# Optimization experiments

Measured on AMD Instinct MI355X. Metric: run time of the kernel, lower is better.

Reference implementation:

```python
import jax, jax.numpy as jnp
import numpy as np
from jax import lax

OBS, ACT, H, VOX = 2264, 32, 4096, 216  # voxel tail is 6*6*6


def _conv3d(v, w, b):
    # v: [1,1,6,6,6], w: [1,1,3,3,3] (OIDHW), SAME padding, stride 1
    y = lax.conv_general_dilated(v, w, window_strides=(1, 1, 1), padding='SAME',
                                 dimension_numbers=('NCDHW', 'OIDHW', 'NCDHW'))
    return jax.nn.relu(y + b.reshape(1, -1, 1, 1, 1))


def setup_inputs() -> dict:
    key = jax.random.key(0)
    ks = jax.random.split(key, 24)
    s = 0.05
    inp = {'x': jax.random.normal(ks[0], (1, OBS), dtype=jnp.float32)}
    # six Conv3d(1,1,3) kernels + biases
    for i in range(6):
        inp[f'cw{i}'] = jax.random.normal(ks[1 + i], (1, 1, 3, 3, 3), dtype=jnp.float32) * s
        inp[f'cb{i}'] = jax.random.normal(ks[7 + i], (1,), dtype=jnp.float32) * s
    # MLP: Linear(OBS->H), Linear(H->H), Linear(H->ACT); torch layout W:[out,in]
    inp['W0'] = jax.random.normal(ks[13], (H, OBS), dtype=jnp.float32) * 0.02
    inp['b0'] = jnp.zeros((H,), jnp.float32)
    inp['W1'] = jax.random.normal(ks[14], (H, H), dtype=jnp.float32) * 0.02
    inp['b1'] = jnp.zeros((H,), jnp.float32)
    inp['W2'] = jax.random.normal(ks[15], (ACT, H), dtype=jnp.float32) * 0.02
    inp['b2'] = jnp.zeros((ACT,), jnp.float32)
    # default transformations (in_shift=0, in_scale=1, out_shift=0, out_scale=1)
    inp['in_shift'] = jnp.zeros((OBS,), jnp.float32)
    inp['in_scale'] = jnp.ones((OBS,), jnp.float32)
    inp['out_shift'] = jnp.zeros((ACT,), jnp.float32)
    inp['out_scale'] = jnp.ones((ACT,), jnp.float32)
    return inp


def reference(x, cw0, cw1, cw2, cw3, cw4, cw5, cb0, cb1, cb2, cb3, cb4, cb5,
              W0, b0, W1, b1, W2, b2, in_shift, in_scale, out_shift, out_scale):
    v = x[:, -VOX:].reshape(1, 1, 6, 6, 6)
    for w, b in ((cw0, cb0), (cw1, cb1), (cw2, cb2), (cw3, cb3), (cw4, cb4), (cw5, cb5)):
        v = _conv3d(v, w, b)
    out = jnp.concatenate([x[:, :-VOX], v.reshape(1, VOX)], axis=1)
    out = (out - in_shift) / (in_scale + 1e-8)
    out = jnp.tanh(out @ W0.T + b0)
    out = jnp.tanh(out @ W1.T + b1)
    out = out @ W2.T + b2
    return out * out_scale + out_shift
```

## Files before the change

### kernel.cpp

```cpp
#include <hip/hip_runtime.h>
#include <math.h>

#define OBS 2264
#define ACT 32
#define HID 4096
#define VOX 216
#define PRE (OBS - VOX)
#define N4_OBS (OBS / 4)
#define N4_HID (HID / 4)
#define NB 256
#define NT 1024
#define RPB 16
#define RPG 4

__global__ __launch_bounds__(NT) void fused0_kernel(
    const float* __restrict__ x,
    const float* __restrict__ cw0, const float* __restrict__ cb0,
    const float* __restrict__ cw1, const float* __restrict__ cb1,
    const float* __restrict__ cw2, const float* __restrict__ cb2,
    const float* __restrict__ cw3, const float* __restrict__ cb3,
    const float* __restrict__ cw4, const float* __restrict__ cb4,
    const float* __restrict__ cw5, const float* __restrict__ cb5,
    const float* __restrict__ in_shift, const float* __restrict__ in_scale,
    const float* __restrict__ W0, const float* __restrict__ b0,
    float* __restrict__ h0)
{
    __shared__ float skw[6][27];
    __shared__ float skb[6];
    __shared__ float vbA[VOX], vbB[VOX];
    __shared__ __align__(16) float su[OBS];
    __shared__ float part[4][RPG][4];

    const int tid = threadIdx.x;

    if (tid < 162) {
        const float* srcw = tid < 27  ? cw0
                          : tid < 54  ? cw1
                          : tid < 81  ? cw2
                          : tid < 108 ? cw3
                          : tid < 135 ? cw4 : cw5;
        const int base = tid < 27  ? 0
                       : tid < 54  ? 27
                       : tid < 81  ? 54
                       : tid < 108 ? 81
                       : tid < 135 ? 108 : 135;
        reinterpret_cast<float*>(skw)[tid] = srcw[tid - base];
    } else if (tid >= 192 && tid < 198) {
        const float* srcb = tid == 192 ? cb0
                          : tid == 193 ? cb1
                          : tid == 194 ? cb2
                          : tid == 195 ? cb3
                          : tid == 196 ? cb4 : cb5;
        skb[tid - 192] = srcb[0];
    }
    if (tid < VOX) vbA[tid] = x[PRE + tid];
    __syncthreads();

    const int d = tid / 36;
    const int h = (tid / 6) % 6;
    const int w = tid % 6;

#define CONV_LAYER(L, SRC, DST)                                              \
    if (tid < VOX) {                                                         \
        float acc = skb[L];                                                  \
        _Pragma("unroll") for (int kd = 0; kd < 3; ++kd) {                   \
            const int dd = d + kd - 1;                                       \
            if (dd >= 0 && dd <= 5) {                                        \
                _Pragma("unroll") for (int kh = 0; kh < 3; ++kh) {           \
                    const int hh = h + kh - 1;                               \
                    if (hh >= 0 && hh <= 5) {                                \
                        _Pragma("unroll") for (int kw2 = 0; kw2 < 3; ++kw2) {\
                            const int ww = w + kw2 - 1;                      \
                            if (ww >= 0 && ww <= 5)                          \
                                acc += skw[L][kd * 9 + kh * 3 + kw2]         \
                                     * SRC[dd * 36 + hh * 6 + ww];           \
                        }                                                    \
                    }                                                        \
                }                                                            \
            }                                                                \
        }                                                                    \
        DST[tid] = fmaxf(acc, 0.f);                                          \
    }                                                                        \
    __syncthreads();

    CONV_LAYER(0, vbA, vbB)
    CONV_LAYER(1, vbB, vbA)
    CONV_LAYER(2, vbA, vbB)
    CONV_LAYER(3, vbB, vbA)
    CONV_LAYER(4, vbA, vbB)
    CONV_LAYER(5, vbB, vbA)
#undef CONV_LAYER

    for (int i = tid; i < OBS; i += NT) {
        const float val = (i < PRE) ? x[i] : vbA[i - PRE];
        su[i] = (val - in_shift[i]) / (in_scale[i] + 1e-8f);
    }
    __syncthreads();

    const int g = tid >> 8;
    const int t = tid & 255;
    const int r0 = blockIdx.x * RPB + g * RPG;
    const float4* __restrict__ su4 = reinterpret_cast<const float4*>(su);
    const float4* __restrict__ W4  = reinterpret_cast<const float4*>(W0);

    float accs[RPG] = {0.f, 0.f, 0.f, 0.f};
    for (int j = t; j < N4_OBS; j += 256) {
        const float4 uv = su4[j];
        #pragma unroll
        for (int r = 0; r < RPG; ++r) {
            const float4 wv = W4[(size_t)(r0 + r) * N4_OBS + j];
            accs[r] += wv.x * uv.x + wv.y * uv.y + wv.z * uv.z + wv.w * uv.w;
        }
    }
    #pragma unroll
    for (int r = 0; r < RPG; ++r) {
        float a = accs[r];
        #pragma unroll
        for (int off = 32; off > 0; off >>= 1) a += __shfl_down(a, off, 64);
        if ((t & 63) == 0) part[g][r][t >> 6] = a;
    }
    __syncthreads();
    if (t < RPG) {
        const float s = part[g][t][0] + part[g][t][1] + part[g][t][2]
                      + part[g][t][3] + b0[r0 + t];
        h0[r0 + t] = tanhf(s);
    }
}

__global__ __launch_bounds__(NT) void gemv1_kernel(
    const float* __restrict__ W, const float* __restrict__ b,
    const float* __restrict__ u, float* __restrict__ out)
{
    __shared__ __align__(16) float sh[HID];
    __shared__ float part[4][RPG][4];

    const int tid = threadIdx.x;

    reinterpret_cast<float4*>(sh)[tid] =
        reinterpret_cast<const float4*>(u)[tid];
    __syncthreads();

    const int g = tid >> 8;
    const int t = tid & 255;
    const int r0 = blockIdx.x * RPB + g * RPG;
    const float4* __restrict__ u4 = reinterpret_cast<const float4*>(sh);
    const float4* __restrict__ W4 = reinterpret_cast<const float4*>(W);

    float accs[RPG] = {0.f, 0.f, 0.f, 0.f};
    for (int j = t; j < N4_HID; j += 256) {
        const float4 uv = u4[j];
        #pragma unroll
        for (int r = 0; r < RPG; ++r) {
            const float4 wv = W4[(size_t)(r0 + r) * N4_HID + j];
            accs[r] += wv.x * uv.x + wv.y * uv.y + wv.z * uv.z + wv.w * uv.w;
        }
    }
    #pragma unroll
    for (int r = 0; r < RPG; ++r) {
        float a = accs[r];
        #pragma unroll
        for (int off = 32; off > 0; off >>= 1) a += __shfl_down(a, off, 64);
        if ((t & 63) == 0) part[g][r][t >> 6] = a;
    }
    __syncthreads();
    if (t < RPG) {
        const float s = part[g][t][0] + part[g][t][1] + part[g][t][2]
                      + part[g][t][3] + b[r0 + t];
        out[r0 + t] = tanhf(s);
    }
}

__global__ __launch_bounds__(NT) void gemv_out_kernel(
    const float* __restrict__ W, const float* __restrict__ b,
    const float* __restrict__ u,
    const float* __restrict__ oscale, const float* __restrict__ oshift,
    float* __restrict__ out)
{
    const int row = blockIdx.x;
    const int tid = threadIdx.x;
    const float4* __restrict__ Wr =
        reinterpret_cast<const float4*>(W + (size_t)row * HID);
    const float4* __restrict__ u4 = reinterpret_cast<const float4*>(u);

    const float4 wv = Wr[tid];
    const float4 uv = u4[tid];
    float a = wv.x * uv.x + wv.y * uv.y + wv.z * uv.z + wv.w * uv.w;

    #pragma unroll
    for (int off = 32; off > 0; off >>= 1) a += __shfl_down(a, off, 64);

    __shared__ float part16[16];
    if ((tid & 63) == 0) part16[tid >> 6] = a;
    __syncthreads();
    if (tid == 0) {
        float s = b[row];
        #pragma unroll
        for (int i = 0; i < 16; ++i) s += part16[i];
        out[row] = s * oscale[row] + oshift[row];
    }
}

extern "C" void kernel_launch(void* const* d_in, const int* in_sizes, int n_in,
                              void* d_out, int out_size, void* d_ws, size_t ws_size,
                              hipStream_t stream) {
    const float* x = (const float*)d_in[0];

    const float* cw[6];
    const float* cb[6];
    if (in_sizes[2] == 1) {
        for (int i = 0; i < 6; ++i) {
            cw[i] = (const float*)d_in[1 + 2 * i];
            cb[i] = (const float*)d_in[2 + 2 * i];
        }
    } else {
        for (int i = 0; i < 6; ++i) {
            cw[i] = (const float*)d_in[1 + i];
            cb[i] = (const float*)d_in[7 + i];
        }
    }
    const float* W0       = (const float*)d_in[13];
    const float* b0       = (const float*)d_in[14];
    const float* W1       = (const float*)d_in[15];
    const float* b1       = (const float*)d_in[16];
    const float* W2       = (const float*)d_in[17];
    const float* b2       = (const float*)d_in[18];
    const float* in_shift = (const float*)d_in[19];
    const float* in_scale = (const float*)d_in[20];
    const float* oshift   = (const float*)d_in[21];
    const float* oscale   = (const float*)d_in[22];

    float* ws = (float*)d_ws;
    float* h0 = ws;
    float* h1 = ws + HID;
    float* y  = (float*)d_out;

    fused0_kernel<<<NB, NT, 0, stream>>>(
        x, cw[0], cb[0], cw[1], cb[1], cw[2], cb[2],
        cw[3], cb[3], cw[4], cb[4], cw[5], cb[5],
        in_shift, in_scale, W0, b0, h0);

    gemv1_kernel<<<NB, NT, 0, stream>>>(W1, b1, h0, h1);
    gemv_out_kernel<<<ACT, NT, 0, stream>>>(W2, b2, h1, oscale, oshift, y);
}
```

Measured before the change: 40.88 us.

## Prefetch W1 into cache during conv stage using half the threads

Splits fused0's threads in two. Half of them (512 threads) prefetch each block's W1 slice with dummy loads during the conv and normalisation phases, so the slice is warmed in the L2/MALL caches before gemv1 reads it. The other half now do the W0 GEMV with 8 rows per group instead of 4. This overlaps part of the second layer's weight traffic with the latency-bound conv chain, at the cost of fewer threads on the first GEMV and of depending on the cached data surviving until the next kernel.

```diff
diff --git a/kernel.cpp b/kernel.cpp
--- a/kernel.cpp
+++ b/kernel.cpp
@@ -11,7 +11,7 @@
 #define NB 256
 #define NT 1024
 #define RPB 16
-#define RPG 4
+#define RPG 8
 
 __global__ __launch_bounds__(NT) void fused0_kernel(
     const float* __restrict__ x,
@@ -23,15 +23,29 @@
     const float* __restrict__ cw5, const float* __restrict__ cb5,
     const float* __restrict__ in_shift, const float* __restrict__ in_scale,
     const float* __restrict__ W0, const float* __restrict__ b0,
+    const float* __restrict__ W1,
     float* __restrict__ h0)
 {
     __shared__ float skw[6][27];
     __shared__ float skb[6];
     __shared__ float vbA[VOX], vbB[VOX];
     __shared__ __align__(16) float su[OBS];
-    __shared__ float part[4][RPG][4];
+    __shared__ float part[2][RPG][4];
 
     const int tid = threadIdx.x;
+
+    const float4* __restrict__ W1p =
+        reinterpret_cast<const float4*>(W1) + (size_t)blockIdx.x * RPB * N4_HID;
+    const int ptid = tid - 512;
+    float4 dead = {0.f, 0.f, 0.f, 0.f};
+#define PREFETCH_SEG(S)                                                      \
+    if (tid >= 512) {                                                        \
+        const int base = (S) * 2048 + ptid * 4;                              \
+        _Pragma("unroll") for (int k = 0; k < 4; ++k) {                      \
+            const float4 v = W1p[base + k];                                  \
+            dead.x += v.x; dead.y += v.y; dead.z += v.z; dead.w += v.w;      \
+        }                                                                    \
+    }
 
     if (tid < 162) {
         const float* srcw = tid < 27  ? cw0
@@ -54,6 +68,7 @@
         skb[tid - 192] = srcb[0];
     }
     if (tid < VOX) vbA[tid] = x[PRE + tid];
+    PREFETCH_SEG(0)
     __syncthreads();
 
     const int d = tid / 36;
@@ -81,6 +96,7 @@
         }                                                                    \
         DST[tid] = fmaxf(acc, 0.f);                                          \
     }                                                                        \
+    PREFETCH_SEG(1 + (L))                                                    \
     __syncthreads();
 
     CONV_LAYER(0, vbA, vbB)
@@ -91,39 +107,53 @@
     CONV_LAYER(5, vbB, vbA)
 #undef CONV_LAYER
 
-    for (int i = tid; i < OBS; i += NT) {
-        const float val = (i < PRE) ? x[i] : vbA[i - PRE];
-        su[i] = (val - in_shift[i]) / (in_scale[i] + 1e-8f);
-    }
-    __syncthreads();
-
-    const int g = tid >> 8;
-    const int t = tid & 255;
-    const int r0 = blockIdx.x * RPB + g * RPG;
-    const float4* __restrict__ su4 = reinterpret_cast<const float4*>(su);
-    const float4* __restrict__ W4  = reinterpret_cast<const float4*>(W0);
-
-    float accs[RPG] = {0.f, 0.f, 0.f, 0.f};
-    for (int j = t; j < N4_OBS; j += 256) {
-        const float4 uv = su4[j];
+    if (tid < 512) {
+        for (int i = tid; i < OBS; i += 512) {
+            const float val = (i < PRE) ? x[i] : vbA[i - PRE];
+            su[i] = (val - in_shift[i]) / (in_scale[i] + 1e-8f);
+        }
+    }
+    PREFETCH_SEG(7)
+    asm volatile("" :: "v"(dead.x), "v"(dead.y), "v"(dead.z), "v"(dead.w));
+#undef PREFETCH_SEG
+    __syncthreads();
+
+    if (tid < 512) {
+        const int g = tid >> 8;
+        const int t = tid & 255;
+        const int r0 = blockIdx.x * RPB + g * RPG;
+        const float4* __restrict__ su4 = reinterpret_cast<const float4*>(su);
+        const float4* __restrict__ W4  = reinterpret_cast<const float4*>(W0);
+
+        float accs[RPG];
+        #pragma unroll
+        for (int r = 0; r < RPG; ++r) accs[r] = 0.f;
+        for (int j = t; j < N4_OBS; j += 256) {
+            const float4 uv = su4[j];
+            #pragma unroll
+            for (int r = 0; r < RPG; ++r) {
+                const float4 wv = W4[(size_t)(r0 + r) * N4_OBS + j];
+                accs[r] += wv.x * uv.x + wv.y * uv.y + wv.z * uv.z + wv.w * uv.w;
+            }
+        }
         #pragma unroll
         for (int r = 0; r < RPG; ++r) {
-            const float4 wv = W4[(size_t)(r0 + r) * N4_OBS + j];
-            accs[r] += wv.x * uv.x + wv.y * uv.y + wv.z * uv.z + wv.w * uv.w;
-        }
-    }
-    #pragma unroll
-    for (int r = 0; r < RPG; ++r) {
-        float a = accs[r];
-        #pragma unroll
-        for (int off = 32; off > 0; off >>= 1) a += __shfl_down(a, off, 64);
-        if ((t & 63) == 0) part[g][r][t >> 6] = a;
-    }
-    __syncthreads();
-    if (t < RPG) {
-        const float s = part[g][t][0] + part[g][t][1] + part[g][t][2]
-                      + part[g][t][3] + b0[r0 + t];
-        h0[r0 + t] = tanhf(s);
+            float a = accs[r];
+            #pragma unroll
+            for (int off = 32; off > 0; off >>= 1) a += __shfl_down(a, off, 64);
+            if ((t & 63) == 0) part[g][r][t >> 6] = a;
+        }
+    }
+    __syncthreads();
+    if (tid < 512) {
+        const int g = tid >> 8;
+        const int t = tid & 255;
+        const int r0 = blockIdx.x * RPB + g * RPG;
+        if (t < RPG) {
+            const float s = part[g][t][0] + part[g][t][1] + part[g][t][2]
+                          + part[g][t][3] + b0[r0 + t];
+            h0[r0 + t] = tanhf(s);
+        }
     }
 }
 
@@ -132,7 +162,7 @@
     const float* __restrict__ u, float* __restrict__ out)
 {
     __shared__ __align__(16) float sh[HID];
-    __shared__ float part[4][RPG][4];
+    __shared__ float part[4][4][4];
 
     const int tid = threadIdx.x;
 
@@ -142,28 +172,28 @@
 
     const int g = tid >> 8;
     const int t = tid & 255;
-    const int r0 = blockIdx.x * RPB + g * RPG;
+    const int r0 = blockIdx.x * RPB + g * 4;
     const float4* __restrict__ u4 = reinterpret_cast<const float4*>(sh);
     const float4* __restrict__ W4 = reinterpret_cast<const float4*>(W);
 
-    float accs[RPG] = {0.f, 0.f, 0.f, 0.f};
+    float accs[4] = {0.f, 0.f, 0.f, 0.f};
     for (int j = t; j < N4_HID; j += 256) {
         const float4 uv = u4[j];
         #pragma unroll
-        for (int r = 0; r < RPG; ++r) {
+        for (int r = 0; r < 4; ++r) {
             const float4 wv = W4[(size_t)(r0 + r) * N4_HID + j];
             accs[r] += wv.x * uv.x + wv.y * uv.y + wv.z * uv.z + wv.w * uv.w;
         }
     }
     #pragma unroll
-    for (int r = 0; r < RPG; ++r) {
+    for (int r = 0; r < 4; ++r) {
         float a = accs[r];
         #pragma unroll
         for (int off = 32; off > 0; off >>= 1) a += __shfl_down(a, off, 64);
         if ((t & 63) == 0) part[g][r][t >> 6] = a;
     }
     __syncthreads();
-    if (t < RPG) {
+    if (t < 4) {
         const float s = part[g][t][0] + part[g][t][1] + part[g][t][2]
                       + part[g][t][3] + b[r0 + t];
         out[r0 + t] = tanhf(s);
@@ -237,7 +267,7 @@
     fused0_kernel<<<NB, NT, 0, stream>>>(
         x, cw[0], cb[0], cw[1], cb[1], cw[2], cb[2],
         cw[3], cb[3], cw[4], cb[4], cw[5], cb[5],
-        in_shift, in_scale, W0, b0, h0);
+        in_shift, in_scale, W0, b0, W1, h0);
 
     gemv1_kernel<<<NB, NT, 0, stream>>>(W1, b1, h0, h1);
     gemv_out_kernel<<<ACT, NT, 0, stream>>>(W2, b2, h1, oscale, oshift, y);
```

Measured after the change: 43.91 us. 1.07x slower.
